# Kernel tuning notes

Measured on AMD Instinct MI355X. Metric: run time of the kernel, lower is better.

Reference implementation:

```python
import jax, jax.numpy as jnp
import numpy as np

# Module hyperparameters (match init_kwargs)
E, H = 16, 8          # embedding_dim, n_head
DI, DO = 8, 8         # dim_in, dim_out (voices)
F = 48                # num_frames_in = num_frames_out = max_num_frames
L_IN, L_OUT = F * DI, F * DO
SZ_B = 4              # batch size (q has SZ_B * H leading dim)


def _expand(mat):
    # mat: (F, F, E, H) -> (L_IN, L_OUT, E, H), block expansion over voices
    e = jnp.tile(mat, (1, DI, 1, 1))                 # (F, DI*F, E, H)
    f = e.reshape(DI * F, F, E, H)                   # (L_IN, F, E, H)
    g = jnp.transpose(f, (1, 0, 2, 3))               # (F, L_IN, E, H)
    h = jnp.tile(g, (1, DO, 1, 1))                   # (F, DO*L_IN, E, H)
    ret = jnp.transpose(h.reshape(DO * F, DI * F, E, H), (1, 0, 2, 3))
    return ret[:L_IN, :L_OUT]


def _prepare_r_time(inp, is_future):
    # inp: (F, E, H). Skewing trick via pad + tile + reshape (faithful to torch).
    a = jnp.concatenate([inp, jnp.full((1, E, H), -111.0, inp.dtype)], axis=0)  # (F+1, E, H)
    b = jnp.tile(a[None], (F, 1, 1, 1))              # (F, F+1, E, H)
    c = b.reshape(F + 1, F, E, H)
    d = c[:F] if is_future else jnp.transpose(c[:F], (1, 0, 2, 3))  # (F, F, E, H)
    return _expand(d)


def _preprocess(r_voice, e_past, e_future):
    one = jnp.ones((F, F), r_voice.dtype)
    mask_past = jnp.broadcast_to(jnp.tril(one)[:, :, None, None], (F, F, E, H))
    mask_future = jnp.broadcast_to(jnp.triu(one, 1)[:, :, None, None], (F, F, E, H))
    r_voice_rep = jnp.tile(r_voice, (F, F, 1, 1))    # (L_IN, L_OUT, E, H)
    r_time = (_expand(mask_past) * _prepare_r_time(e_past, False)
              + _expand(mask_future) * _prepare_r_time(e_future, True))
    return r_voice_rep, r_time


def setup_inputs() -> dict:
    key = jax.random.key(0)
    k1, k2, k3, k4 = jax.random.split(key, 4)
    return {
        "q": jax.random.normal(k1, (SZ_B * H, L_IN, E), jnp.float32),
        "flipped_masks": jnp.zeros((1,), jnp.int32),  # unused by forward
        "r_voice": jax.random.normal(k2, (DI, DO, E, H), jnp.float32),
        "e_past": jax.random.normal(k3, (F, E, H), jnp.float32),
        "e_future": jax.random.normal(k4, (F, E, H), jnp.float32),
    }


def reference(q, flipped_masks, r_voice, e_past, e_future):
    rv, rt = _preprocess(r_voice, e_past, e_future)
    # torch: permute(3,0,1,2) then repeat over batch -> (b*H, L, M, E) with index b*H + h.
    # Equivalent without the batch repeat: reshape q to (b, H, L, E) and einsum over heads.
    rv = jnp.transpose(rv, (3, 0, 1, 2))             # (H, L_IN, L_OUT, E)
    rt = jnp.transpose(rt, (3, 0, 1, 2))
    qb = q.reshape(SZ_B, H, L_IN, E)
    # use_voice_attention=True: rel_attn_instrument + rel_attn_time (single fused einsum)
    rel = jnp.einsum('bhld,hlmd->bhlm', qb, rv + rt)
    return rel.reshape(SZ_B * H, L_IN, L_OUT)
```

## Files before the change

### kernel.cpp

```cpp
#include <hip/hip_runtime.h>
#include <hip/hip_bf16.h>

#define E_DIM 16
#define H_DIM 8
#define F_DIM 48
#define L_IN 384
#define L_OUT 384
#define SZ_B 4

#define NCHUNK 8
#define ROWS_PER_BLOCK 48
#define FI_PER 6
#define TSTRIDE 20

typedef float f32x4 __attribute__((ext_vector_type(4)));

__global__ __launch_bounds__(512)
void bsa_fused_kernel(const float* __restrict__ q,
                      const float* __restrict__ r_voice,
                      const float* __restrict__ e_past,
                      const float* __restrict__ e_future,
                      float* __restrict__ out) {
    const int chunk = blockIdx.x;
    const int bh    = blockIdx.y;
    const int h     = bh & (H_DIM - 1);
    const int t     = threadIdx.x;
    const int w     = t >> 6;
    const int lane  = t & 63;

    __shared__ __attribute__((aligned(16))) float tabs[160 * TSTRIDE];
    __shared__ __attribute__((aligned(16))) float qs[ROWS_PER_BLOCK * E_DIM];
    __shared__ __attribute__((aligned(16))) float scratch[8 * 64];

    for (int i = t; i < F_DIM * E_DIM; i += 512) {
        const int f = i >> 4, d = i & 15;
        tabs[f * TSTRIDE + d]           = e_past [(size_t)i * H_DIM + h];
        tabs[(F_DIM + f) * TSTRIDE + d] = e_future[(size_t)i * H_DIM + h];
    }
    for (int i = t; i < 64 * E_DIM; i += 512) {
        const int r = i >> 4, d = i & 15;
        tabs[(96 + r) * TSTRIDE + d] = r_voice[(size_t)i * H_DIM + h];
    }
    for (int i = t; i < ROWS_PER_BLOCK * E_DIM; i += 512)
        qs[i] = q[((size_t)bh * L_IN + chunk * ROWS_PER_BLOCK) * E_DIM + i];
    __syncthreads();

    float* wscratch = &scratch[w * 64];

    for (int j = 0; j < FI_PER; ++j) {
        const int lrow = w * FI_PER + j;
        const int l    = chunk * ROWS_PER_BLOCK + lrow;
        const int fi   = l >> 3;
        const int vi   = l & 7;

        int r;
        if (lane < 48) {
            r = (lane <= fi) ? (fi - lane) : (F_DIM + lane - fi);
        } else {
            int vj = (lane - 48) & 7;
            r = 96 + vi * 8 + vj;
        }
        const f32x4* qv = (const f32x4*)&qs[lrow * E_DIM];
        const f32x4* tv = (const f32x4*)&tabs[r * TSTRIDE];
        f32x4 acc = qv[0] * tv[0] + qv[1] * tv[1] + qv[2] * tv[2] + qv[3] * tv[3];
        const float s = acc.x + acc.y + acc.z + acc.w;
        if (lane < 56) wscratch[lane] = s;
        asm volatile("s_waitcnt lgkmcnt(0)" ::: "memory");
        __builtin_amdgcn_wave_barrier();

        float* orow = out + ((size_t)bh * L_IN + l) * L_OUT;
        #pragma unroll
        for (int rr = 0; rr < 2; ++rr) {
            const int jj = rr * 64 + lane;
            if (jj < 96) {
                const float tval = wscratch[jj >> 1];
                const f32x4 vv = *(const f32x4*)&wscratch[48 + 4 * (jj & 1)];
                f32x4 o;
                o.x = tval + vv.x; o.y = tval + vv.y;
                o.z = tval + vv.z; o.w = tval + vv.w;
                *(f32x4*)(orow + 4 * jj) = o;
            }
        }
        __builtin_amdgcn_wave_barrier();
    }
}

extern "C" void kernel_launch(void* const* d_in, const int* in_sizes, int n_in,
                              void* d_out, int out_size, void* d_ws, size_t ws_size,
                              hipStream_t stream) {
    const float* q        = (const float*)d_in[0];
    const float* r_voice  = (const float*)d_in[2];
    const float* e_past   = (const float*)d_in[3];
    const float* e_future = (const float*)d_in[4];
    float* out = (float*)d_out;

    dim3 grid(NCHUNK, SZ_B * H_DIM);
    bsa_fused_kernel<<<grid, dim3(512), 0, stream>>>(q, r_voice, e_past, e_future, out);
}
```

Baseline: 11.79 us.

## Split fused kernel into dot-product kernel and separate output expansion kernel

Splits the single fused kernel into two launches. The first computes the per-row time and voice dot products into a workspace buffer. The second is a flat elementwise kernel that expands those values into the full output with one vec4 store per thread. The aim is to spread the output write over many more threads and blocks instead of 256 blocks with serial per-wave rows. In exchange it adds a second launch and a round trip through global memory for the intermediate values.

```diff
diff --git a/kernel.cpp b/kernel.cpp
--- a/kernel.cpp
+++ b/kernel.cpp
@@ -10,17 +10,17 @@
 
 #define NCHUNK 8
 #define ROWS_PER_BLOCK 48
-#define FI_PER 6
+#define ROWS_PER_WAVE 6
 #define TSTRIDE 20
 
 typedef float f32x4 __attribute__((ext_vector_type(4)));
 
 __global__ __launch_bounds__(512)
-void bsa_fused_kernel(const float* __restrict__ q,
-                      const float* __restrict__ r_voice,
-                      const float* __restrict__ e_past,
-                      const float* __restrict__ e_future,
-                      float* __restrict__ out) {
+void bsa_dots_kernel(const float* __restrict__ q,
+                     const float* __restrict__ r_voice,
+                     const float* __restrict__ e_past,
+                     const float* __restrict__ e_future,
+                     float* __restrict__ tv_ws) {
     const int chunk = blockIdx.x;
     const int bh    = blockIdx.y;
     const int h     = bh & (H_DIM - 1);
@@ -30,7 +30,6 @@
 
     __shared__ __attribute__((aligned(16))) float tabs[160 * TSTRIDE];
     __shared__ __attribute__((aligned(16))) float qs[ROWS_PER_BLOCK * E_DIM];
-    __shared__ __attribute__((aligned(16))) float scratch[8 * 64];
 
     for (int i = t; i < F_DIM * E_DIM; i += 512) {
         const int f = i >> 4, d = i & 15;
@@ -45,44 +44,39 @@
         qs[i] = q[((size_t)bh * L_IN + chunk * ROWS_PER_BLOCK) * E_DIM + i];
     __syncthreads();
 
-    float* wscratch = &scratch[w * 64];
-
-    for (int j = 0; j < FI_PER; ++j) {
-        const int lrow = w * FI_PER + j;
+    #pragma unroll
+    for (int j = 0; j < ROWS_PER_WAVE; ++j) {
+        const int lrow = w * ROWS_PER_WAVE + j;
         const int l    = chunk * ROWS_PER_BLOCK + lrow;
         const int fi   = l >> 3;
         const int vi   = l & 7;
-
         int r;
         if (lane < 48) {
             r = (lane <= fi) ? (fi - lane) : (F_DIM + lane - fi);
         } else {
-            int vj = (lane - 48) & 7;
-            r = 96 + vi * 8 + vj;
+            r = 96 + vi * 8 + ((lane - 48) & 7);
         }
         const f32x4* qv = (const f32x4*)&qs[lrow * E_DIM];
         const f32x4* tv = (const f32x4*)&tabs[r * TSTRIDE];
         f32x4 acc = qv[0] * tv[0] + qv[1] * tv[1] + qv[2] * tv[2] + qv[3] * tv[3];
         const float s = acc.x + acc.y + acc.z + acc.w;
-        if (lane < 56) wscratch[lane] = s;
-        asm volatile("s_waitcnt lgkmcnt(0)" ::: "memory");
-        __builtin_amdgcn_wave_barrier();
+        tv_ws[((size_t)bh * L_IN + l) * 64 + lane] = s;
+    }
+}
 
-        float* orow = out + ((size_t)bh * L_IN + l) * L_OUT;
-        #pragma unroll
-        for (int rr = 0; rr < 2; ++rr) {
-            const int jj = rr * 64 + lane;
-            if (jj < 96) {
-                const float tval = wscratch[jj >> 1];
-                const f32x4 vv = *(const f32x4*)&wscratch[48 + 4 * (jj & 1)];
-                f32x4 o;
-                o.x = tval + vv.x; o.y = tval + vv.y;
-                o.z = tval + vv.z; o.w = tval + vv.w;
-                *(f32x4*)(orow + 4 * jj) = o;
-            }
-        }
-        __builtin_amdgcn_wave_barrier();
-    }
+__global__ __launch_bounds__(256)
+void bsa_expand_kernel(const float* __restrict__ tv_ws,
+                       float* __restrict__ out) {
+    const int g   = blockIdx.x * 256 + threadIdx.x;
+    const int row = g / 96;
+    const int jj  = g - row * 96;
+    const float* base = tv_ws + (size_t)row * 64;
+    const float tval = base[jj >> 1];
+    const f32x4 vv = *(const f32x4*)&base[48 + 4 * (jj & 1)];
+    f32x4 o;
+    o.x = tval + vv.x; o.y = tval + vv.y;
+    o.z = tval + vv.z; o.w = tval + vv.w;
+    *(f32x4*)(out + (size_t)4 * g) = o;
 }
 
 extern "C" void kernel_launch(void* const* d_in, const int* in_sizes, int n_in,
@@ -92,8 +86,12 @@
     const float* r_voice  = (const float*)d_in[2];
     const float* e_past   = (const float*)d_in[3];
     const float* e_future = (const float*)d_in[4];
-    float* out = (float*)d_out;
+    float* tv_ws = (float*)d_ws;
+    float* out   = (float*)d_out;
 
-    dim3 grid(NCHUNK, SZ_B * H_DIM);
-    bsa_fused_kernel<<<grid, dim3(512), 0, stream>>>(q, r_voice, e_past, e_future, out);
+    bsa_dots_kernel<<<dim3(NCHUNK, SZ_B * H_DIM), dim3(512), 0, stream>>>(
+        q, r_voice, e_past, e_future, tv_ws);
+
+    const int total_vec4 = SZ_B * H_DIM * L_IN * (L_OUT / 4);
+    bsa_expand_kernel<<<dim3(total_vec4 / 256), dim3(256), 0, stream>>>(tv_ws, out);
 }
```

Result: slower. 15.53 us (+31.7%).
